# Kernel optimization log

Hardware: AMD Instinct MI355X
Metric: run time of the kernel (lower is better)

## Reference

```python
import math
import jax, jax.numpy as jnp
import numpy as np

N_HEAD = 12

def _alibi_slopes(n):
    def p2(m):
        start = 2 ** (-2 ** (-(math.log2(m) - 3)))
        return [start * start ** i for i in range(m)]
    if math.log2(n).is_integer():
        return p2(n)
    closest = 2 ** math.floor(math.log2(n))
    return p2(closest) + _alibi_slopes(2 * closest)[0::2][: n - closest]


def setup_inputs() -> dict:
    key = jax.random.key(0)
    k1, k2, k3 = jax.random.split(key, 3)
    B, T, C = 2, 2048, 768
    x = jax.random.normal(k1, (B, T, C), dtype=jnp.float32)
    Wqkv = jax.random.normal(k2, (C, 3 * C), dtype=jnp.float32) * 0.02
    bqkv = jnp.zeros((3 * C,), dtype=jnp.float32)
    Wproj = jax.random.normal(k3, (C, C), dtype=jnp.float32) * 0.02
    bproj = jnp.zeros((C,), dtype=jnp.float32)
    return {"x": x, "Wqkv": Wqkv, "bqkv": bqkv, "Wproj": Wproj, "bproj": bproj}


def reference(x, Wqkv, bqkv, Wproj, bproj):
    B, T, C = x.shape
    H = N_HEAD
    D = C // H

    qkv = x @ Wqkv + bqkv                       # (B, T, 3C)
    q, k, v = jnp.split(qkv, 3, axis=-1)
    q = q.reshape(B, T, H, D).transpose(0, 2, 1, 3)  # (B, H, T, D)
    k = k.reshape(B, T, H, D).transpose(0, 2, 1, 3)
    v = v.reshape(B, T, H, D).transpose(0, 2, 1, 3)

    scores = jnp.einsum('bhqd,bhkd->bhqk', q, k) / math.sqrt(D)  # (B,H,T,T)

    # ALiBi: subtract slope * clamp(j - i, 0)
    slopes = jnp.asarray(_alibi_slopes(H), dtype=scores.dtype).reshape(1, H, 1, 1)
    pos = jnp.arange(T)
    rel = jnp.clip(pos[None, :] - pos[:, None], 0)               # (T, T) int
    scores = scores - slopes * rel.astype(scores.dtype)[None, None]

    # causal mask: j > i -> -inf
    causal = pos[None, :] > pos[:, None]
    scores = jnp.where(causal[None, None], -jnp.inf, scores)

    att = jax.nn.softmax(scores, axis=-1)                        # (B,H,T,T)
    y = jnp.einsum('bhqk,bhkd->bhqd', att, v)                    # (B,H,T,D)
    y = y.transpose(0, 2, 1, 3).reshape(B, T, C)
    y = y @ Wproj + bproj
    return (y, att)
```

## Files before the change

### kernel.cpp

```cpp
#include <hip/hip_runtime.h>
#include <math.h>


#define LOG2E 1.4426950408889634f
#define SCALE_LOG2E 0.18033688011112042f

typedef __attribute__((ext_vector_type(8))) short bf16x8;
typedef __attribute__((ext_vector_type(4))) float f32x4;

__device__ __forceinline__ unsigned short f2bf(float f) {
  unsigned int u = __builtin_bit_cast(unsigned int, f);
  u = (u + 0x7fffu + ((u >> 16) & 1u)) >> 16;
  return (unsigned short)u;
}

__global__ void k_convert(const float* __restrict__ in, unsigned short* __restrict__ out, int n4) {
  int i = blockIdx.x * blockDim.x + threadIdx.x;
  int stride = gridDim.x * blockDim.x;
  for (; i < n4; i += stride) {
    float4 v = reinterpret_cast<const float4*>(in)[i];
    ushort4 o;
    o.x = f2bf(v.x); o.y = f2bf(v.y); o.z = f2bf(v.z); o.w = f2bf(v.w);
    reinterpret_cast<ushort4*>(out)[i] = o;
  }
}

__global__ __launch_bounds__(256) void k_transpose_w(const float* __restrict__ in,
                                                     unsigned short* __restrict__ out,
                                                     int K, int N) {
  __shared__ float tile[32][33];
  const int bk = blockIdx.x * 32, bn = blockIdx.y * 32;
  const int tr = threadIdx.x >> 5, tc = threadIdx.x & 31;
#pragma unroll
  for (int i = 0; i < 4; ++i)
    tile[tr + i * 8][tc] = in[(size_t)(bk + tr + i * 8) * N + bn + tc];
  __syncthreads();
#pragma unroll
  for (int i = 0; i < 4; ++i)
    out[(size_t)(bn + tr + i * 8) * K + bk + tc] = f2bf(tile[tc][tr + i * 8]);
}

__global__ __launch_bounds__(256) void k_transpose_v(const unsigned short* __restrict__ in,
                                                     unsigned short* __restrict__ out) {
  __shared__ unsigned short tile[32][34];
  const int bt = blockIdx.x * 32, bd = blockIdx.y * 32;
  const size_t base = (size_t)blockIdx.z * 2048 * 64;
  const int tr = threadIdx.x >> 5, tc = threadIdx.x & 31;
#pragma unroll
  for (int i = 0; i < 4; ++i)
    tile[tr + i * 8][tc] = in[base + (size_t)(bt + tr + i * 8) * 64 + bd + tc];
  __syncthreads();
#pragma unroll
  for (int i = 0; i < 4; ++i)
    out[base + (size_t)(bd + tr + i * 8) * 2048 + bt + tc] = tile[tc][tr + i * 8];
}

__global__ __launch_bounds__(256) void k_gemm(
    const unsigned short* __restrict__ A,
    const unsigned short* __restrict__ Bt,
    const float* __restrict__ bias,
    int M, int N, int K, int mode,
    unsigned short* __restrict__ qb,
    unsigned short* __restrict__ kb,
    unsigned short* __restrict__ vb,
    float* __restrict__ yout)
{
  __shared__ __align__(16) unsigned short As[128 * 64];
  __shared__ __align__(16) unsigned short Bs[128 * 64];
  const int bm = blockIdx.x, bn = blockIdx.y;
  const int tid = threadIdx.x;
  const int lane = tid & 63, wid = tid >> 6;
  const int wr = wid >> 1, wc = wid & 1;
  const int lr = lane & 15, lg = lane >> 4;

  f32x4 acc[4][4] = {};

  for (int k0 = 0; k0 < K; k0 += 64) {
    __syncthreads();
#pragma unroll
    for (int i = 0; i < 4; ++i) {
      int c = tid + i * 256;
      int row = c >> 3, g = c & 7;
      int sw = ((g ^ (row & 7)) * 8);
      *reinterpret_cast<bf16x8*>(&As[row * 64 + sw]) =
          *reinterpret_cast<const bf16x8*>(&A[(size_t)(bm * 128 + row) * K + k0 + g * 8]);
      *reinterpret_cast<bf16x8*>(&Bs[row * 64 + sw]) =
          *reinterpret_cast<const bf16x8*>(&Bt[(size_t)(bn * 128 + row) * K + k0 + g * 8]);
    }
    __syncthreads();
#pragma unroll
    for (int kk = 0; kk < 2; ++kk) {
      const int g = kk * 4 + lg;
      bf16x8 af[4], bfrag[4];
#pragma unroll
      for (int f = 0; f < 4; ++f) {
        int ra = wr * 64 + f * 16 + lr;
        af[f] = *reinterpret_cast<const bf16x8*>(&As[ra * 64 + ((g ^ (ra & 7)) * 8)]);
        int rb = wc * 64 + f * 16 + lr;
        bfrag[f] = *reinterpret_cast<const bf16x8*>(&Bs[rb * 64 + ((g ^ (rb & 7)) * 8)]);
      }
#pragma unroll
      for (int fm = 0; fm < 4; ++fm)
#pragma unroll
        for (int fn = 0; fn < 4; ++fn)
          acc[fm][fn] = __builtin_amdgcn_mfma_f32_16x16x32_bf16(af[fm], bfrag[fn], acc[fm][fn], 0, 0, 0);
    }
  }

#pragma unroll
  for (int fm = 0; fm < 4; ++fm)
#pragma unroll
    for (int fn = 0; fn < 4; ++fn) {
      int col = bn * 128 + wc * 64 + fn * 16 + lr;
      float bi = bias[col];
#pragma unroll
      for (int r = 0; r < 4; ++r) {
        int rowm = bm * 128 + wr * 64 + fm * 16 + lg * 4 + r;
        float val = acc[fm][fn][r] + bi;
        if (mode == 0) {
          int which = col / 768;
          int c = col - which * 768;
          int h = c >> 6, d = c & 63;
          int b = rowm >> 11, t = rowm & 2047;
          size_t bh = (size_t)b * 12 + h;
          unsigned short uv = f2bf(val);
          size_t idx = (bh * 2048 + t) * 64 + d;
          if (which == 0)      qb[idx] = uv;
          else if (which == 1) kb[idx] = uv;
          else                 vb[idx] = uv;
        } else {
          yout[(size_t)rowm * N + col] = val;
        }
      }
    }
}

__global__ __launch_bounds__(256) void k_attn(
    const unsigned short* __restrict__ qb,
    const unsigned short* __restrict__ kb,
    const unsigned short* __restrict__ vT,
    float* __restrict__ att,
    unsigned short* __restrict__ yh)
{
  __shared__ __align__(16) unsigned short Ps[4][16 * 64];

  const int qt = gridDim.x - 1 - blockIdx.x;
  const int bh = blockIdx.y;
  const int tid = threadIdx.x;
  const int lane = tid & 63, wid = tid >> 6;
  const int lr = lane & 15, lg = lane >> 4;

  const unsigned short* Qg = qb + ((size_t)bh * 2048 + qt * 64) * 64;
  const unsigned short* Kg = kb + (size_t)bh * 2048 * 64;
  const unsigned short* Vg = vT + (size_t)bh * 64 * 2048;
  float* attg = att + ((size_t)bh * 2048 + qt * 64) * 2048;

  bf16x8 qf[2];
#pragma unroll
  for (int kk = 0; kk < 2; ++kk)
    qf[kk] = *reinterpret_cast<const bf16x8*>(&Qg[(unsigned)((wid * 16 + lr) * 64 + kk * 32 + lg * 8)]);

  const int qrow_l = wid * 16 + lg * 4;

  float l_r[4] = {0.f, 0.f, 0.f, 0.f};
  for (int kt = 0; kt <= qt; ++kt) {
    f32x4 s[4] = {};
#pragma unroll
    for (int kk = 0; kk < 2; ++kk) {
      const int g = kk * 4 + lg;
#pragma unroll
      for (int fc = 0; fc < 4; ++fc) {
        bf16x8 kf = *reinterpret_cast<const bf16x8*>(
            &Kg[(unsigned)((kt * 64 + fc * 16 + lr) * 64 + g * 8)]);
        s[fc] = __builtin_amdgcn_mfma_f32_16x16x32_bf16(qf[kk], kf, s[fc], 0, 0, 0);
      }
    }
#pragma unroll
    for (int fc = 0; fc < 4; ++fc)
#pragma unroll
      for (int r = 0; r < 4; ++r) {
        bool masked = (kt == qt) && ((fc * 16 + lr) > (qrow_l + r));
        float p = exp2f(s[fc][r] * SCALE_LOG2E);
        l_r[r] += masked ? 0.f : p;
      }
  }
  float rcp_l[4];
#pragma unroll
  for (int r = 0; r < 4; ++r) {
#pragma unroll
    for (int d = 1; d < 16; d <<= 1) l_r[r] += __shfl_xor(l_r[r], d);
    rcp_l[r] = 1.0f / l_r[r];
  }

  f32x4 o[4] = {};
  for (int kt = 0; kt <= qt; ++kt) {
    f32x4 s[4] = {};
#pragma unroll
    for (int kk = 0; kk < 2; ++kk) {
      const int g = kk * 4 + lg;
#pragma unroll
      for (int fc = 0; fc < 4; ++fc) {
        bf16x8 kf = *reinterpret_cast<const bf16x8*>(
            &Kg[(unsigned)((kt * 64 + fc * 16 + lr) * 64 + g * 8)]);
        s[fc] = __builtin_amdgcn_mfma_f32_16x16x32_bf16(qf[kk], kf, s[fc], 0, 0, 0);
      }
    }

#pragma unroll
    for (int fc = 0; fc < 4; ++fc)
#pragma unroll
      for (int r = 0; r < 4; ++r) {
        bool masked = (kt == qt) && ((fc * 16 + lr) > (qrow_l + r));
        float p = masked ? 0.f : exp2f(s[fc][r] * SCALE_LOG2E);
        attg[(size_t)(qrow_l + r) * 2048 + kt * 64 + fc * 16 + lr] = p * rcp_l[r];
        int pr = lg * 4 + r;
        int col = fc * 16 + lr;
        Ps[wid][pr * 64 + (((col >> 3) ^ (pr & 7)) * 8) + (col & 7)] = f2bf(p);
      }

#pragma unroll
    for (int kk = 0; kk < 2; ++kk) {
      const int g = kk * 4 + lg;
      bf16x8 pa = *reinterpret_cast<const bf16x8*>(&Ps[wid][lr * 64 + ((g ^ (lr & 7)) * 8)]);
#pragma unroll
      for (int fc = 0; fc < 4; ++fc) {
        bf16x8 vf = *reinterpret_cast<const bf16x8*>(
            &Vg[(unsigned)((fc * 16 + lr) * 2048 + kt * 64 + g * 8)]);
        o[fc] = __builtin_amdgcn_mfma_f32_16x16x32_bf16(pa, vf, o[fc], 0, 0, 0);
      }
    }
  }

  {
    int W = 2048 - (qt + 1) * 64;
    if (W > 0) {
      int base = (qt + 1) * 64;
      int Wq = W >> 2;
      int n4 = 64 * Wq;
      float4 z = {0.f, 0.f, 0.f, 0.f};
      for (int i = tid; i < n4; i += 256) {
        int row = i / Wq, c4 = i - row * Wq;
        *reinterpret_cast<float4*>(&attg[(size_t)row * 2048 + base + c4 * 4]) = z;
      }
    }
  }

  {
    int b = bh / 12, h = bh - b * 12;
#pragma unroll
    for (int fc = 0; fc < 4; ++fc)
#pragma unroll
      for (int r = 0; r < 4; ++r) {
        int tg = qt * 64 + qrow_l + r;
        yh[((size_t)b * 2048 + tg) * 768 + h * 64 + fc * 16 + lr] = f2bf(o[fc][r] * rcp_l[r]);
      }
  }
}

extern "C" void kernel_launch(void* const* d_in, const int* in_sizes, int n_in,
                              void* d_out, int out_size, void* d_ws, size_t ws_size,
                              hipStream_t stream) {
  const float* x     = (const float*)d_in[0];
  const float* Wqkv  = (const float*)d_in[1];
  const float* bqkv  = (const float*)d_in[2];
  const float* Wproj = (const float*)d_in[3];
  const float* bproj = (const float*)d_in[4];

  float* y   = (float*)d_out;
  float* att = y + (size_t)2 * 2048 * 768;

  char* ws = (char*)d_ws;
  unsigned short* xb     = (unsigned short*)(ws);
  unsigned short* wqkvT  = (unsigned short*)(ws + 6291456);
  unsigned short* wprojT = (unsigned short*)(ws + 9830400);
  unsigned short* qb     = (unsigned short*)(ws + 11010048);
  unsigned short* kb     = (unsigned short*)(ws + 17301504);
  unsigned short* vb     = (unsigned short*)(ws + 23592960);
  unsigned short* yh     = (unsigned short*)(ws + 29884416);
  unsigned short* vT     = xb;

  k_convert<<<1024, 256, 0, stream>>>(x, xb, (2 * 2048 * 768) / 4);
  k_transpose_w<<<dim3(24, 72), 256, 0, stream>>>(Wqkv, wqkvT, 768, 2304);
  k_transpose_w<<<dim3(24, 24), 256, 0, stream>>>(Wproj, wprojT, 768, 768);

  k_gemm<<<dim3(32, 18), 256, 0, stream>>>(xb, wqkvT, bqkv, 4096, 2304, 768, 0,
                                           qb, kb, vb, nullptr);
  k_transpose_v<<<dim3(64, 2, 24), 256, 0, stream>>>(vb, vT);
  k_attn<<<dim3(32, 24), 256, 0, stream>>>(qb, kb, vT, att, yh);
  k_gemm<<<dim3(32, 6), 256, 0, stream>>>(yh, wprojT, bproj, 4096, 768, 768, 1,
                                          nullptr, nullptr, nullptr, y);
}
```

Before: 687.0 us.

## Split attention into single-pass flash kernel plus separate tiled attention-matrix writer

```diff
diff --git a/kernel.cpp b/kernel.cpp
--- a/kernel.cpp
+++ b/kernel.cpp
@@ -2,7 +2,6 @@
 #include <math.h>
 
 
-#define LOG2E 1.4426950408889634f
 #define SCALE_LOG2E 0.18033688011112042f
 
 typedef __attribute__((ext_vector_type(8))) short bf16x8;
@@ -135,36 +134,39 @@
     }
 }
 
-__global__ __launch_bounds__(256) void k_attn(
+__global__ __launch_bounds__(64) void k_flash(
     const unsigned short* __restrict__ qb,
     const unsigned short* __restrict__ kb,
     const unsigned short* __restrict__ vT,
-    float* __restrict__ att,
+    float* __restrict__ rl,
     unsigned short* __restrict__ yh)
 {
-  __shared__ __align__(16) unsigned short Ps[4][16 * 64];
-
-  const int qt = gridDim.x - 1 - blockIdx.x;
+  __shared__ __align__(16) unsigned short Ps[16 * 64];
+
+  const int s = 127 - (int)blockIdx.x;
   const int bh = blockIdx.y;
-  const int tid = threadIdx.x;
-  const int lane = tid & 63, wid = tid >> 6;
+  const int lane = threadIdx.x;
   const int lr = lane & 15, lg = lane >> 4;
 
-  const unsigned short* Qg = qb + ((size_t)bh * 2048 + qt * 64) * 64;
+  const int qrow0 = s * 16;
+  const int ktmax = s >> 2;
+
+  const unsigned short* Qg = qb + ((size_t)bh * 2048 + qrow0) * 64;
   const unsigned short* Kg = kb + (size_t)bh * 2048 * 64;
   const unsigned short* Vg = vT + (size_t)bh * 64 * 2048;
-  float* attg = att + ((size_t)bh * 2048 + qt * 64) * 2048;
 
   bf16x8 qf[2];
 #pragma unroll
   for (int kk = 0; kk < 2; ++kk)
-    qf[kk] = *reinterpret_cast<const bf16x8*>(&Qg[(unsigned)((wid * 16 + lr) * 64 + kk * 32 + lg * 8)]);
-
-  const int qrow_l = wid * 16 + lg * 4;
+    qf[kk] = *reinterpret_cast<const bf16x8*>(&Qg[(unsigned)(lr * 64 + kk * 32 + lg * 8)]);
+
+  const int rloc = (s & 3) * 16 + lg * 4;
 
   float l_r[4] = {0.f, 0.f, 0.f, 0.f};
-  for (int kt = 0; kt <= qt; ++kt) {
-    f32x4 s[4] = {};
+  f32x4 o[4] = {};
+
+  for (int kt = 0; kt <= ktmax; ++kt) {
+    f32x4 sc[4] = {};
 #pragma unroll
     for (int kk = 0; kk < 2; ++kk) {
       const int g = kk * 4 + lg;
@@ -172,56 +174,27 @@
       for (int fc = 0; fc < 4; ++fc) {
         bf16x8 kf = *reinterpret_cast<const bf16x8*>(
             &Kg[(unsigned)((kt * 64 + fc * 16 + lr) * 64 + g * 8)]);
-        s[fc] = __builtin_amdgcn_mfma_f32_16x16x32_bf16(qf[kk], kf, s[fc], 0, 0, 0);
-      }
-    }
+        sc[fc] = __builtin_amdgcn_mfma_f32_16x16x32_bf16(qf[kk], kf, sc[fc], 0, 0, 0);
+      }
+    }
+
+    const bool diag = (kt == ktmax);
 #pragma unroll
     for (int fc = 0; fc < 4; ++fc)
 #pragma unroll
       for (int r = 0; r < 4; ++r) {
-        bool masked = (kt == qt) && ((fc * 16 + lr) > (qrow_l + r));
-        float p = exp2f(s[fc][r] * SCALE_LOG2E);
-        l_r[r] += masked ? 0.f : p;
-      }
-  }
-  float rcp_l[4];
-#pragma unroll
-  for (int r = 0; r < 4; ++r) {
-#pragma unroll
-    for (int d = 1; d < 16; d <<= 1) l_r[r] += __shfl_xor(l_r[r], d);
-    rcp_l[r] = 1.0f / l_r[r];
-  }
-
-  f32x4 o[4] = {};
-  for (int kt = 0; kt <= qt; ++kt) {
-    f32x4 s[4] = {};
+        bool masked = diag && ((fc * 16 + lr) > (rloc + r));
+        float p = masked ? 0.f : exp2f(sc[fc][r] * SCALE_LOG2E);
+        l_r[r] += p;
+        int pr = lg * 4 + r;
+        int col = fc * 16 + lr;
+        Ps[pr * 64 + (((col >> 3) ^ (pr & 7)) * 8) + (col & 7)] = f2bf(p);
+      }
+
 #pragma unroll
     for (int kk = 0; kk < 2; ++kk) {
       const int g = kk * 4 + lg;
-#pragma unroll
-      for (int fc = 0; fc < 4; ++fc) {
-        bf16x8 kf = *reinterpret_cast<const bf16x8*>(
-            &Kg[(unsigned)((kt * 64 + fc * 16 + lr) * 64 + g * 8)]);
-        s[fc] = __builtin_amdgcn_mfma_f32_16x16x32_bf16(qf[kk], kf, s[fc], 0, 0, 0);
-      }
-    }
-
-#pragma unroll
-    for (int fc = 0; fc < 4; ++fc)
-#pragma unroll
-      for (int r = 0; r < 4; ++r) {
-        bool masked = (kt == qt) && ((fc * 16 + lr) > (qrow_l + r));
-        float p = masked ? 0.f : exp2f(s[fc][r] * SCALE_LOG2E);
-        attg[(size_t)(qrow_l + r) * 2048 + kt * 64 + fc * 16 + lr] = p * rcp_l[r];
-        int pr = lg * 4 + r;
-        int col = fc * 16 + lr;
-        Ps[wid][pr * 64 + (((col >> 3) ^ (pr & 7)) * 8) + (col & 7)] = f2bf(p);
-      }
-
-#pragma unroll
-    for (int kk = 0; kk < 2; ++kk) {
-      const int g = kk * 4 + lg;
-      bf16x8 pa = *reinterpret_cast<const bf16x8*>(&Ps[wid][lr * 64 + ((g ^ (lr & 7)) * 8)]);
+      bf16x8 pa = *reinterpret_cast<const bf16x8*>(&Ps[lr * 64 + ((g ^ (lr & 7)) * 8)]);
 #pragma unroll
       for (int fc = 0; fc < 4; ++fc) {
         bf16x8 vf = *reinterpret_cast<const bf16x8*>(
@@ -231,18 +204,18 @@
     }
   }
 
-  {
-    int W = 2048 - (qt + 1) * 64;
-    if (W > 0) {
-      int base = (qt + 1) * 64;
-      int Wq = W >> 2;
-      int n4 = 64 * Wq;
-      float4 z = {0.f, 0.f, 0.f, 0.f};
-      for (int i = tid; i < n4; i += 256) {
-        int row = i / Wq, c4 = i - row * Wq;
-        *reinterpret_cast<float4*>(&attg[(size_t)row * 2048 + base + c4 * 4]) = z;
-      }
-    }
+  float rcp_l[4];
+#pragma unroll
+  for (int r = 0; r < 4; ++r) {
+#pragma unroll
+    for (int d = 1; d < 16; d <<= 1) l_r[r] += __shfl_xor(l_r[r], d);
+    rcp_l[r] = 1.0f / l_r[r];
+  }
+
+  if (lr == 0) {
+#pragma unroll
+    for (int r = 0; r < 4; ++r)
+      rl[(size_t)bh * 2048 + qrow0 + lg * 4 + r] = rcp_l[r];
   }
 
   {
@@ -251,10 +224,66 @@
     for (int fc = 0; fc < 4; ++fc)
 #pragma unroll
       for (int r = 0; r < 4; ++r) {
-        int tg = qt * 64 + qrow_l + r;
+        int tg = qrow0 + lg * 4 + r;
         yh[((size_t)b * 2048 + tg) * 768 + h * 64 + fc * 16 + lr] = f2bf(o[fc][r] * rcp_l[r]);
       }
   }
+}
+
+__global__ __launch_bounds__(256) void k_attmat(
+    const unsigned short* __restrict__ qb,
+    const unsigned short* __restrict__ kb,
+    const float* __restrict__ rl,
+    float* __restrict__ att)
+{
+  const int kt = blockIdx.x, qt = blockIdx.y, bh = blockIdx.z;
+  const int tid = threadIdx.x;
+  float* attg = att + ((size_t)bh * 2048 + qt * 64) * 2048 + kt * 64;
+
+  if (kt > qt) {
+    int row = tid >> 2, seg = tid & 3;
+    float4 z = {0.f, 0.f, 0.f, 0.f};
+#pragma unroll
+    for (int j = 0; j < 4; ++j)
+      *reinterpret_cast<float4*>(&attg[(size_t)row * 2048 + seg * 16 + j * 4]) = z;
+    return;
+  }
+
+  const int lane = tid & 63, wid = tid >> 6;
+  const int lr = lane & 15, lg = lane >> 4;
+
+  const unsigned short* Qg = qb + ((size_t)bh * 2048 + qt * 64 + wid * 16) * 64;
+  const unsigned short* Kg = kb + ((size_t)bh * 2048 + kt * 64) * 64;
+
+  bf16x8 qf[2];
+#pragma unroll
+  for (int kk = 0; kk < 2; ++kk)
+    qf[kk] = *reinterpret_cast<const bf16x8*>(&Qg[(unsigned)(lr * 64 + kk * 32 + lg * 8)]);
+
+  f32x4 sc[4] = {};
+#pragma unroll
+  for (int kk = 0; kk < 2; ++kk) {
+    const int g = kk * 4 + lg;
+#pragma unroll
+    for (int fc = 0; fc < 4; ++fc) {
+      bf16x8 kf = *reinterpret_cast<const bf16x8*>(
+          &Kg[(unsigned)((fc * 16 + lr) * 64 + g * 8)]);
+      sc[fc] = __builtin_amdgcn_mfma_f32_16x16x32_bf16(qf[kk], kf, sc[fc], 0, 0, 0);
+    }
+  }
+
+  const int rloc = wid * 16 + lg * 4;
+  f32x4 rcp = *reinterpret_cast<const f32x4*>(&rl[(size_t)bh * 2048 + qt * 64 + rloc]);
+
+  const bool diag = (kt == qt);
+#pragma unroll
+  for (int fc = 0; fc < 4; ++fc)
+#pragma unroll
+    for (int r = 0; r < 4; ++r) {
+      bool masked = diag && ((fc * 16 + lr) > (rloc + r));
+      float p = masked ? 0.f : exp2f(sc[fc][r] * SCALE_LOG2E) * rcp[r];
+      attg[(size_t)(rloc + r) * 2048 + fc * 16 + lr] = p;
+    }
 }
 
 extern "C" void kernel_launch(void* const* d_in, const int* in_sizes, int n_in,
@@ -277,6 +306,7 @@
   unsigned short* kb     = (unsigned short*)(ws + 17301504);
   unsigned short* vb     = (unsigned short*)(ws + 23592960);
   unsigned short* yh     = (unsigned short*)(ws + 29884416);
+  float*          rlbuf  = (float*)(ws + 36175872);
   unsigned short* vT     = xb;
 
   k_convert<<<1024, 256, 0, stream>>>(x, xb, (2 * 2048 * 768) / 4);
@@ -286,7 +316,9 @@
   k_gemm<<<dim3(32, 18), 256, 0, stream>>>(xb, wqkvT, bqkv, 4096, 2304, 768, 0,
                                            qb, kb, vb, nullptr);
   k_transpose_v<<<dim3(64, 2, 24), 256, 0, stream>>>(vb, vT);
-  k_attn<<<dim3(32, 24), 256, 0, stream>>>(qb, kb, vT, att, yh);
+
+  k_flash<<<dim3(128, 24), 64, 0, stream>>>(qb, kb, vT, rlbuf, yh);
   k_gemm<<<dim3(32, 6), 256, 0, stream>>>(yh, wprojT, bproj, 4096, 768, 768, 1,
                                           nullptr, nullptr, nullptr, y);
-}
+  k_attmat<<<dim3(32, 32, 24), 256, 0, stream>>>(qb, kb, rlbuf, att);
+}
```

After: 716.7 us. +4.3%, slower.
